# Kernel optimization log

Hardware: AMD Instinct MI355X
Metric: run time of the kernel (lower is better)

## Reference

```python
import jax, jax.numpy as jnp
import numpy as np
from jax import lax

# geomloss SamplesLoss('sinkhorn', p=2, blur=0.01, scaling=0.9) semantics:
# debiased Sinkhorn divergence S_eps(a,b) = OT_eps(x,y) - 0.5*OT_eps(x,x) - 0.5*OT_eps(y,y)
# with cost C = ||x-y||^2 / 2, uniform weights, and epsilon annealing from
# diameter^p down to blur^p with ratio scaling^p.
P = 2
BLUR = 0.01
SCALING = 0.9
DIAMETER = 8.0  # static upper bound on point-cloud spread for randn data

def _eps_schedule():
    scales = []
    s = DIAMETER
    while s > BLUR:
        scales.append(s)
        s *= SCALING
    scales.append(BLUR)
    return jnp.asarray(np.array(scales, np.float32) ** P)

def _sqcost(x, y):
    # x: [B,N,D], y: [B,M,D] -> C[B,N,M] = 0.5*||x_i-y_j||^2
    x2 = jnp.sum(x * x, -1)[:, :, None]
    y2 = jnp.sum(y * y, -1)[:, None, :]
    return 0.5 * (x2 + y2 - 2.0 * jnp.einsum('bnd,bmd->bnm', x, y))

def _sinkhorn_divergence(x, y):
    B, N, _ = x.shape
    M = y.shape[1]
    logN = jnp.log(jnp.float32(N))
    logM = jnp.log(jnp.float32(M))
    eps_list = _eps_schedule()

    Cxy = _sqcost(x, y)          # [B,N,M]
    Cyx = jnp.swapaxes(Cxy, 1, 2)
    Cxx = _sqcost(x, x)
    Cyy = _sqcost(y, y)

    def softmin(eps, C, h, logw):
        # -eps * log sum_j exp(log w_j + (h_j - C_ij)/eps)
        return -eps * jax.nn.logsumexp((h[:, None, :] - C) / eps - logw, axis=-1)

    # potentials computed under envelope theorem (no grad through iterations)
    Cxy_d, Cyx_d = lax.stop_gradient(Cxy), lax.stop_gradient(Cyx)
    Cxx_d, Cyy_d = lax.stop_gradient(Cxx), lax.stop_gradient(Cyy)

    z = jnp.zeros((B, N), x.dtype)
    zy = jnp.zeros((B, M), x.dtype)

    def body(carry, eps):
        f, g, fx, gy = carry
        ft = softmin(eps, Cxy_d, g, logM)
        gt = softmin(eps, Cyx_d, f, logN)
        f, g = 0.5 * (f + ft), 0.5 * (g + gt)
        fx = 0.5 * (fx + softmin(eps, Cxx_d, fx, logN))
        gy = 0.5 * (gy + softmin(eps, Cyy_d, gy, logM))
        return (f, g, fx, gy), None

    (f, g, fx, gy), _ = lax.scan(body, (z, zy, z, zy), eps_list)

    # last extrapolation at target eps, differentiable w.r.t. the costs
    eps_t = eps_list[-1]
    f_fin = softmin(eps_t, Cxy, lax.stop_gradient(g), logM)
    g_fin = softmin(eps_t, Cyx, lax.stop_gradient(f), logN)
    fx_fin = softmin(eps_t, Cxx, lax.stop_gradient(fx), logN)
    gy_fin = softmin(eps_t, Cyy, lax.stop_gradient(gy), logM)

    # S = <a, f - fx> + <b, g - gy>, uniform weights
    return jnp.mean(f_fin - fx_fin, axis=-1) + jnp.mean(g_fin - gy_fin, axis=-1)  # [B]


def setup_inputs() -> dict:
    key = jax.random.key(0)
    k1, k2 = jax.random.split(key)
    B, N, D = 8, 2048, 3
    p1 = jax.random.normal(k1, (B, N, D), dtype=jnp.float32)
    p2 = jax.random.normal(k2, (B, N, D), dtype=jnp.float32)
    return {"p1": p1, "p2": p2}


def reference(p1, p2):
    # EMD_Loss.forward: mean over batch of per-sample Sinkhorn divergences
    return jnp.mean(_sinkhorn_divergence(p1, p2))
```

## Files before the change

kernel.cpp:

```cpp
#include <hip/hip_runtime.h>
#include <math.h>

#define NPTS 2048
#define NB 8

typedef float v2f __attribute__((ext_vector_type(2)));

__device__ __forceinline__ float wexp2(float v) { return __builtin_amdgcn_exp2f(v); }
__device__ __forceinline__ v2f fma2(v2f a, v2f b, v2f c) {
  return __builtin_elementwise_fma(a, b, c);
}
__device__ __forceinline__ v2f max2(v2f a, v2f b) {
  return __builtin_elementwise_max(a, b);
}

__global__ __launch_bounds__(256) void emd_init(const float* __restrict__ x,
                                                const float* __restrict__ y,
                                                float4* __restrict__ x4,
                                                float4* __restrict__ y4,
                                                float* __restrict__ pot0,
                                                float* __restrict__ out) {
  int t = blockIdx.x * blockDim.x + threadIdx.x;
  if (t < NB * NPTS) {
    float a0 = x[3 * t], a1 = x[3 * t + 1], a2 = x[3 * t + 2];
    x4[t] = make_float4(a0, a1, a2, 0.5f * (a0 * a0 + a1 * a1 + a2 * a2));
    float b0 = y[3 * t], b1 = y[3 * t + 1], b2 = y[3 * t + 2];
    y4[t] = make_float4(b0, b1, b2, 0.5f * (b0 * b0 + b1 * b1 + b2 * b2));
  }
  pot0[t] = 0.0f;
  if (t == 0) out[0] = 0.0f;
}

__global__ __launch_bounds__(1024, 8) void emd_sweep_boot(
    const float4* __restrict__ x4, const float4* __restrict__ y4,
    const float* __restrict__ pot_in, float* __restrict__ pot_out,
    float* __restrict__ amax_out, float c, float neg_eps_ln2, float eps_logM) {
  __shared__ union {
    struct { float4 A[NPTS / 2]; float4 B[NPTS / 2]; } cp;
    struct { float m[16][128]; float l[16][128]; } mg;
  } sh;

  int blk = blockIdx.x;
  int mat = blk >> 7;
  int b = (blk >> 4) & 7;
  int rg = blk & 15;
  int tid = threadIdx.x;
  int lane = tid & 63;
  int w = tid >> 6;

  const float4* rowp = (mat & 1) ? y4 : x4;
  const float4* colp = (mat == 0 || mat == 3) ? y4 : x4;
  int hidx = (mat < 2) ? (mat ^ 1) : mat;
  const float* h = pot_in + (hidx * NB + b) * NPTS;
  const float4* colb = colp + b * NPTS;

  {
    float4 q0 = colb[2 * tid];
    float4 q1 = colb[2 * tid + 1];
    float2 hv = ((const float2*)h)[tid];
    sh.cp.A[tid] = make_float4(q0.x, q1.x, q0.y, q1.y);
    sh.cp.B[tid] = make_float4(q0.z, q1.z, (hv.x - q0.w) * c, (hv.y - q1.w) * c);
  }
  __syncthreads();

  int rowbase = rg * 128;
  const float4* rowb = rowp + b * NPTS + rowbase;

  v2f xs0[2], xs1[2], xs2[2];
  float m[2], l[2];
#pragma unroll
  for (int r = 0; r < 2; ++r) {
    float4 p = rowb[r * 64 + lane];
    float a0 = p.x * c, a1 = p.y * c, a2 = p.z * c;
    xs0[r] = (v2f){a0, a0};
    xs1[r] = (v2f){a1, a1};
    xs2[r] = (v2f){a2, a2};
    m[r] = -INFINITY;
    l[r] = 0.0f;
  }

  int p0 = w * 64;
  for (int tp = 0; tp < 64; tp += 4) {
    float4 A[4], B[4];
#pragma unroll
    for (int j = 0; j < 4; ++j) {
      A[j] = sh.cp.A[p0 + tp + j];
      B[j] = sh.cp.B[p0 + tp + j];
    }
#pragma unroll
    for (int r = 0; r < 2; ++r) {
      v2f s2[4];
#pragma unroll
      for (int j = 0; j < 4; ++j) {
        v2f qx = {A[j].x, A[j].y};
        v2f qy = {A[j].z, A[j].w};
        v2f qz = {B[j].x, B[j].y};
        v2f qw = {B[j].z, B[j].w};
        s2[j] = fma2(xs0[r], qx, fma2(xs1[r], qy, fma2(xs2[r], qz, qw)));
      }
      v2f t0 = max2(s2[0], s2[1]);
      v2f t1 = max2(s2[2], s2[3]);
      v2f u = max2(t0, t1);
      float mt = fmaxf(u.x, u.y);
      float mn = fmaxf(m[r], mt);
      v2f mn2 = {mn, mn};
      v2f acc = {0.0f, 0.0f};
#pragma unroll
      for (int j = 0; j < 4; ++j) {
        v2f d = s2[j] - mn2;
        v2f e;
        e.x = wexp2(d.x);
        e.y = wexp2(d.y);
        acc += e;
      }
      l[r] = fmaf(l[r], wexp2(m[r] - mn), acc.x + acc.y);
      m[r] = mn;
    }
  }

  __syncthreads();
#pragma unroll
  for (int r = 0; r < 2; ++r) {
    sh.mg.m[w][r * 64 + lane] = m[r];
    sh.mg.l[w][r * 64 + lane] = l[r];
  }
  __syncthreads();

  if (w < 2) {
    int row = w * 64 + lane;
    float M = sh.mg.m[0][row];
#pragma unroll
    for (int q = 1; q < 16; ++q) M = fmaxf(M, sh.mg.m[q][row]);
    float L = 0.0f;
#pragma unroll
    for (int q = 0; q < 16; ++q)
      L += sh.mg.l[q][row] * wexp2(sh.mg.m[q][row] - M);
    float pw = rowb[row].w;
    float res = pw + neg_eps_ln2 * (M + log2f(L)) + eps_logM;
    float invc = -neg_eps_ln2;
    int idx = (mat * NB + b) * NPTS + rowbase + row;
    amax_out[idx] = M * invc;
    pot_out[idx] = 0.5f * (pot_in[idx] + res);
  }
}

__global__ __launch_bounds__(1024, 8) void emd_partial(
    const float4* __restrict__ x4, const float4* __restrict__ y4,
    const float* __restrict__ pot_in, const float* __restrict__ am_in,
    float* __restrict__ Lp, float c) {
  __shared__ union {
    struct { float4 A[512]; float4 B[512]; } cp;
    float lbuf[16][256];
  } sh;

  int blk = blockIdx.x;
  int mat = blk >> 7;
  int b = (blk >> 4) & 7;
  int rg = (blk >> 1) & 7;
  int cg = blk & 1;
  int tid = threadIdx.x;
  int lane = tid & 63;
  int w = tid >> 6;

  const float4* rowp = (mat & 1) ? y4 : x4;
  const float4* colp = (mat == 0 || mat == 3) ? y4 : x4;
  int hidx = (mat < 2) ? (mat ^ 1) : mat;
  const float* h = pot_in + (hidx * NB + b) * NPTS;
  const float4* colb = colp + b * NPTS;

  if (tid < 512) {
    int jg = cg * 1024 + 2 * tid;
    float4 q0 = colb[jg];
    float4 q1 = colb[jg + 1];
    float2 hv = *(const float2*)(h + jg);
    sh.cp.A[tid] = make_float4(q0.x, q1.x, q0.y, q1.y);
    sh.cp.B[tid] = make_float4(q0.z, q1.z, (hv.x - q0.w) * c, (hv.y - q1.w) * c);
  }
  __syncthreads();

  int rowbase = rg * 256;
  const float4* rowb = rowp + b * NPTS + rowbase;
  const float* amrow = am_in + (mat * NB + b) * NPTS + rowbase;

  v2f xs0[4], xs1[4], xs2[4], mref2[4], acc[4];
#pragma unroll
  for (int r = 0; r < 4; ++r) {
    float4 p = rowb[r * 64 + lane];
    float a0 = p.x * c, a1 = p.y * c, a2 = p.z * c;
    xs0[r] = (v2f){a0, a0};
    xs1[r] = (v2f){a1, a1};
    xs2[r] = (v2f){a2, a2};
    float mr = amrow[r * 64 + lane] * c;
    mref2[r] = (v2f){mr, mr};
    acc[r] = (v2f){0.0f, 0.0f};
  }

  int p0 = w * 32;
  for (int tp = 0; tp < 32; ++tp) {
    float4 A = sh.cp.A[p0 + tp];
    float4 B = sh.cp.B[p0 + tp];
    v2f qx = {A.x, A.y};
    v2f qy = {A.z, A.w};
    v2f qz = {B.x, B.y};
    v2f qw = {B.z, B.w};
#pragma unroll
    for (int r = 0; r < 4; ++r) {
      v2f s2 = fma2(xs0[r], qx, fma2(xs1[r], qy, fma2(xs2[r], qz, qw)));
      v2f d = s2 - mref2[r];
      v2f e;
      e.x = wexp2(d.x);
      e.y = wexp2(d.y);
      acc[r] += e;
    }
  }

  __syncthreads();
#pragma unroll
  for (int r = 0; r < 4; ++r)
    sh.lbuf[w][r * 64 + lane] = acc[r].x + acc[r].y;
  __syncthreads();

  if (w < 4) {
    int row = w * 64 + lane;
    float L = sh.lbuf[0][row];
#pragma unroll
    for (int q = 1; q < 16; ++q) L += sh.lbuf[q][row];
    Lp[2 * ((mat * NB + b) * NPTS) + cg * NPTS + rowbase + row] = L;
  }
}

template <bool FINAL>
__global__ __launch_bounds__(256) void emd_merge(
    const float4* __restrict__ x4, const float4* __restrict__ y4,
    const float* __restrict__ Lp, const float* __restrict__ am_in,
    const float* __restrict__ pot_in, float* __restrict__ pot_out,
    float* __restrict__ am_out, float* __restrict__ out,
    float invc, float elM) {
  int t = blockIdx.x * 256 + threadIdx.x;
  int mat = t >> 14;
  int b = (t >> 11) & 7;
  int i = t & 2047;
  const float4* rowp = (mat & 1) ? y4 : x4;
  float pw = rowp[b * NPTS + i].w;
  int base = (mat * NB + b) * NPTS;
  float L = Lp[2 * base + i] + Lp[2 * base + NPTS + i];
  float lse = fmaf(log2f(L), invc, am_in[base + i]);
  float res = pw - lse + elM;
  if (FINAL) {
    float sign = (mat < 2) ? 1.0f : -1.0f;
    float val = sign * res * (1.0f / (float)(NB * NPTS));
#pragma unroll
    for (int off = 32; off; off >>= 1) val += __shfl_xor(val, off);
    if ((threadIdx.x & 63) == 0) atomicAdd(out, val);
  } else {
    pot_out[base + i] = 0.5f * (pot_in[base + i] + res);
    am_out[base + i] = lse;
  }
}

extern "C" void kernel_launch(void* const* d_in, const int* in_sizes, int n_in,
                              void* d_out, int out_size, void* d_ws, size_t ws_size,
                              hipStream_t stream) {
  const float* x = (const float*)d_in[0];
  const float* y = (const float*)d_in[1];
  float* out = (float*)d_out;

  char* ws = (char*)d_ws;
  float4* x4 = (float4*)ws;
  float4* y4 = (float4*)(ws + 262144);
  float* pot = (float*)(ws + 524288);
  float* am[2];
  am[0] = (float*)(ws + 1048576);
  am[1] = (float*)(ws + 1310720);
  float* Lp = (float*)(ws + 1572864);

  emd_init<<<256, 256, 0, stream>>>(x, y, x4, y4, pot, out);

  float eps_arr[80];
  int ne = 0;
  double s = 8.0;
  while (s > 0.01) {
    float sf = (float)s;
    eps_arr[ne++] = sf * sf;
    s *= 0.9;
  }
  {
    float bf = 0.01f;
    eps_arr[ne++] = bf * bf;
  }

  const double LOG2E = 1.4426950408889634;
  const double LN2 = 0.6931471805599453;
  const double LOG2048 = 7.624618986159398;

  {
    float eps = eps_arr[0];
    float c = (float)(LOG2E / (double)eps);
    float nel = (float)(-(double)eps * LN2);
    float elM = (float)((double)eps * LOG2048);
    emd_sweep_boot<<<512, 1024, 0, stream>>>(x4, y4, pot, pot + 65536,
                                             am[0], c, nel, elM);
  }

  for (int k = 1; k < ne; ++k) {
    float eps = eps_arr[k];
    float c = (float)(LOG2E / (double)eps);
    float invc = (float)((double)eps * LN2);
    float elM = (float)((double)eps * LOG2048);
    float* potIn = pot + (k % 2) * 65536;
    float* potOut = pot + ((k + 1) % 2) * 65536;
    const float* amIn = am[(k - 1) % 2];
    float* amOut = am[k % 2];
    emd_partial<<<512, 1024, 0, stream>>>(x4, y4, potIn, amIn, Lp, c);
    emd_merge<false><<<256, 256, 0, stream>>>(x4, y4, Lp, amIn, potIn, potOut,
                                              amOut, nullptr, invc, elM);
  }

  {
    float eps = eps_arr[ne - 1];
    float c = (float)(LOG2E / (double)eps);
    float invc = (float)((double)eps * LN2);
    float elM = (float)((double)eps * LOG2048);
    float* potIn = pot + (ne % 2) * 65536;
    const float* amIn = am[(ne - 1) % 2];
    emd_partial<<<512, 1024, 0, stream>>>(x4, y4, potIn, amIn, Lp, c);
    emd_merge<true><<<256, 256, 0, stream>>>(x4, y4, Lp, amIn, nullptr, nullptr,
                                             nullptr, out, invc, elM);
  }
}
```

Baseline: 1.574 ms.

## Fuse merge step into next sweep's column loading, removing per-iteration merge kernel

Removes the separate merge kernel after each Sinkhorn iteration. The next sweep kernel now decodes the previous iteration's partial sums while loading its column potentials, and one row-group block writes the updated potential and log-sum-exp reference. The loop needs a triple-buffered reference array and double-buffered partial sums, and only a small finalize kernel stays at the end. This halves the kernel launches per iteration, but every block repeats the log2 decode work for its columns.

Result: faster. 1.493 ms (-5.2%).

```diff
diff --git a/kernel.cpp b/kernel.cpp
--- a/kernel.cpp
+++ b/kernel.cpp
@@ -34,7 +34,8 @@
 __global__ __launch_bounds__(1024, 8) void emd_sweep_boot(
     const float4* __restrict__ x4, const float4* __restrict__ y4,
     const float* __restrict__ pot_in, float* __restrict__ pot_out,
-    float* __restrict__ amax_out, float c, float neg_eps_ln2, float eps_logM) {
+    float* __restrict__ am0, float* __restrict__ am1,
+    float c, float neg_eps_ln2, float eps_logM) {
   __shared__ union {
     struct { float4 A[NPTS / 2]; float4 B[NPTS / 2]; } cp;
     struct { float m[16][128]; float l[16][128]; } mg;
@@ -139,15 +140,22 @@
     float res = pw + neg_eps_ln2 * (M + log2f(L)) + eps_logM;
     float invc = -neg_eps_ln2;
     int idx = (mat * NB + b) * NPTS + rowbase + row;
-    amax_out[idx] = M * invc;
-    pot_out[idx] = 0.5f * (pot_in[idx] + res);
-  }
-}
-
-__global__ __launch_bounds__(1024, 8) void emd_partial(
+    am0[idx] = M * invc;
+    am1[idx] = (M + log2f(L)) * invc;
+    pot_out[idx] = 0.5f * (0.0f + res);
+  }
+}
+
+template <bool DECODE>
+__global__ __launch_bounds__(1024, 8) void emd_sweep_ref(
     const float4* __restrict__ x4, const float4* __restrict__ y4,
-    const float* __restrict__ pot_in, const float* __restrict__ am_in,
-    float* __restrict__ Lp, float c) {
+    const float* __restrict__ pot_in, float* __restrict__ pot_out,
+    const float* __restrict__ amRows,
+    const float* __restrict__ amDec,
+    float* __restrict__ amWr,
+    const float* __restrict__ LpIn,
+    float* __restrict__ LpOut,
+    float c, float invc_prev, float elM_prev) {
   __shared__ union {
     struct { float4 A[512]; float4 B[512]; } cp;
     float lbuf[16][256];
@@ -165,22 +173,36 @@
   const float4* rowp = (mat & 1) ? y4 : x4;
   const float4* colp = (mat == 0 || mat == 3) ? y4 : x4;
   int hidx = (mat < 2) ? (mat ^ 1) : mat;
-  const float* h = pot_in + (hidx * NB + b) * NPTS;
+  int hbase = (hidx * NB + b) * NPTS;
   const float4* colb = colp + b * NPTS;
 
   if (tid < 512) {
     int jg = cg * 1024 + 2 * tid;
     float4 q0 = colb[jg];
     float4 q1 = colb[jg + 1];
-    float2 hv = *(const float2*)(h + jg);
+    float2 hv = *(const float2*)(pot_in + hbase + jg);
+    float h0 = hv.x, h1 = hv.y;
+    if (DECODE) {
+      float2 lpa = *(const float2*)(LpIn + 2 * hbase + jg);
+      float2 lpb = *(const float2*)(LpIn + 2 * hbase + NPTS + jg);
+      float2 rd = *(const float2*)(amDec + hbase + jg);
+      float lse0 = fmaf(log2f(lpa.x + lpb.x), invc_prev, rd.x);
+      float lse1 = fmaf(log2f(lpa.y + lpb.y), invc_prev, rd.y);
+      float res0 = q0.w - lse0 + elM_prev;
+      float res1 = q1.w - lse1 + elM_prev;
+      h0 = 0.5f * (h0 + res0);
+      h1 = 0.5f * (h1 + res1);
+      if (rg == 0) *(float2*)(amWr + hbase + jg) = make_float2(lse0, lse1);
+    }
+    if (rg == 0) *(float2*)(pot_out + hbase + jg) = make_float2(h0, h1);
     sh.cp.A[tid] = make_float4(q0.x, q1.x, q0.y, q1.y);
-    sh.cp.B[tid] = make_float4(q0.z, q1.z, (hv.x - q0.w) * c, (hv.y - q1.w) * c);
+    sh.cp.B[tid] = make_float4(q0.z, q1.z, (h0 - q0.w) * c, (h1 - q1.w) * c);
   }
   __syncthreads();
 
   int rowbase = rg * 256;
   const float4* rowb = rowp + b * NPTS + rowbase;
-  const float* amrow = am_in + (mat * NB + b) * NPTS + rowbase;
+  const float* amrow = amRows + (mat * NB + b) * NPTS + rowbase;
 
   v2f xs0[4], xs1[4], xs2[4], mref2[4], acc[4];
 #pragma unroll
@@ -225,37 +247,29 @@
     float L = sh.lbuf[0][row];
 #pragma unroll
     for (int q = 1; q < 16; ++q) L += sh.lbuf[q][row];
-    Lp[2 * ((mat * NB + b) * NPTS) + cg * NPTS + rowbase + row] = L;
-  }
-}
-
-template <bool FINAL>
-__global__ __launch_bounds__(256) void emd_merge(
+    LpOut[2 * ((mat * NB + b) * NPTS) + cg * NPTS + rowbase + row] = L;
+  }
+}
+
+__global__ __launch_bounds__(256) void emd_finalize(
     const float4* __restrict__ x4, const float4* __restrict__ y4,
-    const float* __restrict__ Lp, const float* __restrict__ am_in,
-    const float* __restrict__ pot_in, float* __restrict__ pot_out,
-    float* __restrict__ am_out, float* __restrict__ out,
-    float invc, float elM) {
+    const float* __restrict__ Lp, const float* __restrict__ amR,
+    float* __restrict__ out, float invc_t, float elM_t) {
   int t = blockIdx.x * 256 + threadIdx.x;
   int mat = t >> 14;
   int b = (t >> 11) & 7;
   int i = t & 2047;
-  const float4* rowp = (mat & 1) ? y4 : x4;
-  float pw = rowp[b * NPTS + i].w;
+  const float4* pp = (mat & 1) ? y4 : x4;
+  float pw = pp[b * NPTS + i].w;
   int base = (mat * NB + b) * NPTS;
   float L = Lp[2 * base + i] + Lp[2 * base + NPTS + i];
-  float lse = fmaf(log2f(L), invc, am_in[base + i]);
-  float res = pw - lse + elM;
-  if (FINAL) {
-    float sign = (mat < 2) ? 1.0f : -1.0f;
-    float val = sign * res * (1.0f / (float)(NB * NPTS));
-#pragma unroll
-    for (int off = 32; off; off >>= 1) val += __shfl_xor(val, off);
-    if ((threadIdx.x & 63) == 0) atomicAdd(out, val);
-  } else {
-    pot_out[base + i] = 0.5f * (pot_in[base + i] + res);
-    am_out[base + i] = lse;
-  }
+  float lse = fmaf(log2f(L), invc_t, amR[base + i]);
+  float res = pw - lse + elM_t;
+  float sign = (mat < 2) ? 1.0f : -1.0f;
+  float val = sign * res * (1.0f / (float)(NB * NPTS));
+#pragma unroll
+  for (int off = 32; off; off >>= 1) val += __shfl_xor(val, off);
+  if ((threadIdx.x & 63) == 0) atomicAdd(out, val);
 }
 
 extern "C" void kernel_launch(void* const* d_in, const int* in_sizes, int n_in,
@@ -269,10 +283,13 @@
   float4* x4 = (float4*)ws;
   float4* y4 = (float4*)(ws + 262144);
   float* pot = (float*)(ws + 524288);
-  float* am[2];
+  float* am[3];
   am[0] = (float*)(ws + 1048576);
-  am[1] = (float*)(ws + 1310720);
-  float* Lp = (float*)(ws + 1572864);
+  am[1] = (float*)(ws + 1048576 + 262144);
+  am[2] = (float*)(ws + 1048576 + 524288);
+  float* Lp[2];
+  Lp[0] = (float*)(ws + 1835008);
+  Lp[1] = (float*)(ws + 1835008 + 524288);
 
   emd_init<<<256, 256, 0, stream>>>(x, y, x4, y4, pot, out);
 
@@ -299,32 +316,40 @@
     float nel = (float)(-(double)eps * LN2);
     float elM = (float)((double)eps * LOG2048);
     emd_sweep_boot<<<512, 1024, 0, stream>>>(x4, y4, pot, pot + 65536,
-                                             am[0], c, nel, elM);
-  }
-
-  for (int k = 1; k < ne; ++k) {
-    float eps = eps_arr[k];
+                                             am[0], am[1], c, nel, elM);
+  }
+
+  for (int k = 1; k <= ne; ++k) {
+    int ek = (k < ne) ? k : ne - 1;
+    float eps = eps_arr[ek];
+    float epsp = eps_arr[ek - (k < ne ? 1 : 0)];
     float c = (float)(LOG2E / (double)eps);
-    float invc = (float)((double)eps * LN2);
-    float elM = (float)((double)eps * LOG2048);
+    float invc_p = (float)((double)epsp * LN2);
+    float elM_p = (float)((double)epsp * LOG2048);
+    const float* rowsR = am[(k - 1) % 3];
+    const float* decR = am[(k + 1) % 3];
+    float* wrR = am[k % 3];
     float* potIn = pot + (k % 2) * 65536;
     float* potOut = pot + ((k + 1) % 2) * 65536;
-    const float* amIn = am[(k - 1) % 2];
-    float* amOut = am[k % 2];
-    emd_partial<<<512, 1024, 0, stream>>>(x4, y4, potIn, amIn, Lp, c);
-    emd_merge<false><<<256, 256, 0, stream>>>(x4, y4, Lp, amIn, potIn, potOut,
-                                              amOut, nullptr, invc, elM);
+    float* lpIn = Lp[(k - 1) % 2];
+    float* lpOut = Lp[k % 2];
+    if (k == 1) {
+      emd_sweep_ref<false><<<512, 1024, 0, stream>>>(
+          x4, y4, potIn, potOut, rowsR, decR, wrR, lpIn, lpOut,
+          c, invc_p, elM_p);
+    } else {
+      emd_sweep_ref<true><<<512, 1024, 0, stream>>>(
+          x4, y4, potIn, potOut, rowsR, decR, wrR, lpIn, lpOut,
+          c, invc_p, elM_p);
+    }
   }
 
   {
-    float eps = eps_arr[ne - 1];
-    float c = (float)(LOG2E / (double)eps);
-    float invc = (float)((double)eps * LN2);
-    float elM = (float)((double)eps * LOG2048);
-    float* potIn = pot + (ne % 2) * 65536;
-    const float* amIn = am[(ne - 1) % 2];
-    emd_partial<<<512, 1024, 0, stream>>>(x4, y4, potIn, amIn, Lp, c);
-    emd_merge<true><<<256, 256, 0, stream>>>(x4, y4, Lp, amIn, nullptr, nullptr,
-                                             nullptr, out, invc, elM);
-  }
-}
+    float eps_t = eps_arr[ne - 1];
+    float invc_t = (float)((double)eps_t * LN2);
+    float elM_t = (float)((double)eps_t * LOG2048);
+    emd_finalize<<<256, 256, 0, stream>>>(x4, y4, Lp[ne % 2],
+                                          am[(ne - 1) % 3], out,
+                                          invc_t, elM_t);
+  }
+}
```
